# Kernel optimization log

Measured on AMD Instinct MI355X. Metric: run time of the kernel, lower is better.

The kernel has to match this reference:

```python
import jax, jax.numpy as jnp
import numpy as np

# ---- config (matches init_kwargs) ----
B, N_ENC, COND_REPEAT = 4, 4, 200
BLOCKS, LAYERS_PER = 2, 8
R, S, CC, CLASSES = 128, 128, 64, 256
Q_ZERO = 128
DILATIONS = [2 ** i for i in range(LAYERS_PER)] * BLOCKS  # [1..128, 1..128]
L = len(DILATIONS)


def setup_inputs() -> dict:
    key = jax.random.key(0)
    ks = jax.random.split(key, 12)
    g = lambda k, shape, fan: (jax.random.normal(k, shape, jnp.float32) / np.float32(np.sqrt(fan)))
    return {
        "encodings": jax.random.normal(ks[0], (B, CC, N_ENC), jnp.float32),
        "W_first": g(ks[1], (R, 1, 2), 2.0),            # causal conv 1->R, k=2
        "b_first": jnp.zeros((R,), jnp.float32),
        "Wc": g(ks[2], (L, 2 * R, R, 2), 2.0 * R),       # dilated causal convs R->2R, k=2
        "bc": jnp.zeros((L, 2 * R), jnp.float32),
        "Wcond": g(ks[3], (L, 2 * R, CC), CC),           # per-layer 1x1 cond (no bias)
        "Wres": g(ks[4], (L, R, R), R),                  # per-layer 1x1 residual
        "bres": jnp.zeros((L, R), jnp.float32),
        "Wskip_l": g(ks[5], (L, S, R), R),               # per-layer 1x1 skip
        "bskip_l": jnp.zeros((L, S), jnp.float32),
        "Wskip0": g(ks[6], (S, R), R),                   # top skip_conv
        "bskip0": jnp.zeros((S,), jnp.float32),
        "Wcond_top": g(ks[7], (S, CC), CC),              # top 1x1 cond (no bias)
        "Wfc": g(ks[8], (S, S), S),
        "bfc": jnp.zeros((S,), jnp.float32),
        "Wlogits": g(ks[9], (CLASSES, S), S),
        "blogits": jnp.zeros((CLASSES,), jnp.float32),
    }


def reference(encodings, W_first, b_first, Wc, bc, Wcond, Wres, bres,
              Wskip_l, bskip_l, Wskip0, bskip0, Wcond_top, Wfc, bfc,
              Wlogits, blogits):
    """Autoregressive WaveNet generation with per-layer dilated-conv queues.
    Returns per-step logits [B, CLASSES, T] (sampling uses argmax, method='max')."""
    T = N_ENC * COND_REPEAT
    # each encoding frame conditions cond_repeat consecutive samples
    c_seq = jnp.repeat(encodings, COND_REPEAT, axis=2).transpose(2, 0, 1)  # [T,B,CC]

    def step(carry, c_t):
        sample, fq, queues = carry  # sample:[B] int, fq:[B] (first-conv queue), queues: tuple of [B,R,d_l]
        x = sample.astype(jnp.float32) / 127.5 - 1.0  # mu-law index -> [-1, 1]
        # first causal conv (k=2): past value from queue, current value x
        res = fq[:, None] * W_first[:, 0, 0] + x[:, None] * W_first[:, 0, 1] + b_first  # [B,R]
        skip = res @ Wskip0.T + bskip0  # [B,S]
        new_queues = []
        for l in range(L):  # fixed structural loop over layers
            q = queues[l]  # [B,R,d_l]; q[:,:,0] is the input from d_l steps ago
            z = q[:, :, 0] @ Wc[l, :, :, 0].T + res @ Wc[l, :, :, 1].T + bc[l]  # [B,2R]
            z = z + c_t @ Wcond[l].T
            gate, out = jnp.split(z, 2, axis=1)
            h = jax.nn.sigmoid(gate) * jnp.tanh(out)
            new_queues.append(jnp.concatenate([q[:, :, 1:], res[:, :, None]], axis=2))
            skip = skip + h @ Wskip_l[l].T + bskip_l[l]
            res = res + h @ Wres[l].T + bres[l]  # residual connection
        s = jax.nn.relu(skip) @ Wfc.T + bfc + c_t @ Wcond_top.T
        logits = jax.nn.relu(s) @ Wlogits.T + blogits  # [B,CLASSES]
        new_sample = jnp.argmax(logits, axis=1).astype(jnp.int32)
        return (new_sample, x, tuple(new_queues)), logits

    carry0 = (jnp.full((B,), Q_ZERO, jnp.int32),
              jnp.zeros((B,), jnp.float32),
              tuple(jnp.zeros((B, R, d), jnp.float32) for d in DILATIONS))
    _, logits = jax.lax.scan(step, carry0, c_seq)
    return logits.transpose(1, 2, 0)  # [B, CLASSES, T]
```

## Files before the change

kernel.cpp:

```cpp
#include <hip/hip_runtime.h>


typedef unsigned long long u64;
typedef float f32x4 __attribute__((ext_vector_type(4)));

#define TSTEPS 800
#define CREP 200

#define CTR_OFF 0
#define ABT_OFF 64
#define RESBOX_OFF 4096
#define BOXB 16384
#define SKIPBOX_OFF (RESBOX_OFF + 4 * BOXB)
#define RING_OFF (SKIPBOX_OFF + 4 * BOXB)
#define RINGB 261120
#define WS_END (RING_OFF + 4 * RINGB)

#define SPIN_LIMIT 1048576

static __device__ __forceinline__ void pub64(u64* p, float x, unsigned tag) {
  const u64 v = (u64)__float_as_uint(x) | ((u64)tag << 32);
  asm volatile("global_atomic_swap_x2 %0, %1, off" ::"v"(p), "v"(v) : "memory");
}
static __device__ __forceinline__ u64 poll64(u64* p) {
  u64 old;
  const u64 z = 0;
  asm volatile("global_atomic_add_x2 %0, %1, %2, off sc0\n\ts_waitcnt vmcnt(0)"
               : "=&v"(old) : "v"(p), "v"(z) : "memory");
  return old;
}
static __device__ __forceinline__ void poll4(u64* p, u64& a, u64& b, u64& c, u64& d) {
  const u64 z = 0;
  asm volatile(
      "global_atomic_add_x2 %0, %4, %5, off sc0\n\t"
      "global_atomic_add_x2 %1, %4, %5, off offset:1024 sc0\n\t"
      "global_atomic_add_x2 %2, %4, %5, off offset:2048 sc0\n\t"
      "global_atomic_add_x2 %3, %4, %5, off offset:3072 sc0\n\t"
      "s_waitcnt vmcnt(0)"
      : "=&v"(a), "=&v"(b), "=&v"(c), "=&v"(d)
      : "v"(p), "v"(z)
      : "memory");
}
static __device__ __forceinline__ unsigned ld32(const unsigned* p) {
  return __hip_atomic_load(p, __ATOMIC_RELAXED, __HIP_MEMORY_SCOPE_AGENT);
}
static __device__ __forceinline__ void st32(unsigned* p, unsigned v) {
  __hip_atomic_store(p, v, __ATOMIC_RELAXED, __HIP_MEMORY_SCOPE_AGENT);
}
static __device__ __forceinline__ float spinf(u64* p, unsigned tag, unsigned* abt) {
  int g = 0;
  for (;;) {
    const u64 v = poll64(p);
    if ((unsigned)(v >> 32) == tag) return __uint_as_float((unsigned)v);
    if (((++g) & 255) == 0) {
      if (g > SPIN_LIMIT || ld32(abt)) { st32(abt, 1u); return 0.f; }
    }
  }
}

__global__ void wn_init(unsigned char* ws) {
  uint4 z; z.x = 0; z.y = 0; z.z = 0; z.w = 0;
  uint4* p = (uint4*)ws;
  const int n = WS_END / 16;
  for (int i = blockIdx.x * blockDim.x + threadIdx.x; i < n; i += gridDim.x * blockDim.x)
    p[i] = z;
}

__global__ __launch_bounds__(512, 2) void wn_main(
    const float* __restrict__ enc, const float* __restrict__ Wfirst,
    const float* __restrict__ bfirst, const float* __restrict__ Wc,
    const float* __restrict__ bcv, const float* __restrict__ Wcond,
    const float* __restrict__ Wres, const float* __restrict__ bres,
    const float* __restrict__ Wskip, const float* __restrict__ bskipl,
    const float* __restrict__ Wskip0, const float* __restrict__ bskip0,
    const float* __restrict__ Wct, const float* __restrict__ Wfcw,
    const float* __restrict__ bfc, const float* __restrict__ Wlg,
    const float* __restrict__ blgg, float* __restrict__ dout,
    unsigned char* __restrict__ ws) {
  __shared__ __attribute__((aligned(16))) float wc0L[32768];
  __shared__ __attribute__((aligned(16))) unsigned char smem[14336];
  float* zbS = (float*)smem;
  float* ct2 = (float*)smem;
  float* resS = (float*)(smem + 4096);
  float* zpartS = (float*)(smem + 4608);
  float* ppS = (float*)(smem + 6656);
  float* hS = (float*)(smem + 8704);
  float* rpartS = (float*)(smem + 9216);
  float* skpartS = (float*)(smem + 11264);
  float* pastS = (float*)(smem + 13312);
  float* amaxv = (float*)(smem + 13824);
  int* amaxi = (int*)(smem + 13840);
  int* argixS = (int*)(smem + 13856);
  int* roleS = (int*)(smem + 13872);

  const int tid = threadIdx.x;
  unsigned* abt = (unsigned*)(ws + ABT_OFF);

  if (tid == 0) {
    unsigned xcc;
    asm volatile("s_getreg_b32 %0, hwreg(HW_REG_XCC_ID)" : "=s"(xcc));
    int role = 999;
    if (xcc < 4)
      role = (int)__hip_atomic_fetch_add((unsigned*)(ws + CTR_OFF) + xcc, 1u,
                                         __ATOMIC_RELAXED, __HIP_MEMORY_SCOPE_AGENT);
    roleS[0] = role;
    roleS[1] = (int)xcc;
  }
  __syncthreads();
  const int role = roleS[0];
  const int b = roleS[1];
  if (role >= 17) return;

  const int jz = tid & 255, kh = tid >> 8;
  const int j3 = tid & 127, q3 = tid >> 7;

  if (role < 16) {
    const int l = role;
    const int dl = 1 << (l & 7);
    const int pfx = (l < 8) ? ((1 << l) - 1) : (254 + (1 << (l - 8)));

    f32x4 wc1h[16];
    f32x4 wresq[8];
    {
      const f32x4* wbase = (const f32x4*)(Wc + ((size_t)(l * 256 + jz) * 128 + kh * 64) * 2);
#pragma unroll
      for (int m = 0; m < 16; m++) {
        const f32x4 v0 = wbase[2 * m];
        const f32x4 v1 = wbase[2 * m + 1];
        f32x4 w1;
        w1.x = v0.y; w1.y = v0.w; w1.z = v1.y; w1.w = v1.w;
        wc1h[m] = w1;
      }
      const f32x4* rbase = (const f32x4*)(Wres + (size_t)(l * 128 + j3) * 128 + q3 * 32);
#pragma unroll
      for (int m = 0; m < 8; m++) wresq[m] = rbase[m];
#pragma unroll
      for (int m = 0; m < 16; m++) asm volatile("" : "+v"(wc1h[m]));
#pragma unroll
      for (int m = 0; m < 8; m++) asm volatile("" : "+v"(wresq[m]));
    }
    const float bresv = bres[l * 128 + j3];

    for (int idx = tid; idx < 32768; idx += 512) {
      const int j = idx >> 7, k = idx & 127;
      wc0L[k * 256 + j] = Wc[((size_t)(l * 256 + j) * 128 + k) * 2];
    }

    if (tid < 256) {
      for (int e = 0; e < 4; e++) {
        float a = bcv[l * 256 + tid];
        for (int c = 0; c < 64; c++)
          a = fmaf(enc[(b * 64 + c) * 4 + e], Wcond[((size_t)l * 256 + tid) * 64 + c], a);
        zbS[e * 256 + tid] = a;
      }
    }
    ppS[tid] = 0.f;

    u64* inbox = (u64*)(ws + RESBOX_OFF + (size_t)b * BOXB) + l * 128;
    u64* outbox = (u64*)(ws + RESBOX_OFF + (size_t)b * BOXB) + ((l + 1) & 15) * 128;
    u64* skipbox = (u64*)(ws + SKIPBOX_OFF + (size_t)b * BOXB) + l * 128;
    float* ringf = (float*)(ws + RING_OFF + (size_t)b * RINGB) + pfx * 128;
    const f32x4* wskb = (const f32x4*)(Wskip + (size_t)(l * 128 + j3) * 128 + q3 * 32);
    __syncthreads();

    for (int t = 0; t < TSTEPS; t++) {
      const unsigned want = (unsigned)(t + 1);
      const int e = t / CREP;

      if (tid < 128) resS[tid] = spinf(inbox + tid, want, abt);
      __syncthreads();

      {
        const f32x4* r4 = (const f32x4*)(resS + kh * 64);
        float zp = 0.f;
#pragma unroll
        for (int m = 0; m < 16; m++) {
          const f32x4 r = r4[m];
          const f32x4 w = wc1h[m];
          zp = fmaf(r.x, w.x, zp);
          zp = fmaf(r.y, w.y, zp);
          zp = fmaf(r.z, w.z, zp);
          zp = fmaf(r.w, w.w, zp);
        }
        zpartS[(kh << 8) | jz] = zp;
      }
      __syncthreads();
      if (tid < 128) {
        const float g0 = zpartS[tid] + zpartS[256 + tid] + ppS[tid] + ppS[256 + tid] +
                         zbS[e * 256 + tid];
        const float o0 = zpartS[128 + tid] + zpartS[384 + tid] + ppS[128 + tid] +
                         ppS[384 + tid] + zbS[e * 256 + 128 + tid];
        hS[tid] = (1.f / (1.f + expf(-g0))) * tanhf(o0);
      }
      __syncthreads();

      {
        const f32x4* h4 = (const f32x4*)(hS + q3 * 32);
        float rp2 = 0.f;
#pragma unroll
        for (int m = 0; m < 8; m++) {
          const f32x4 hv = h4[m];
          const f32x4 w = wresq[m];
          rp2 = fmaf(hv.x, w.x, rp2);
          rp2 = fmaf(hv.y, w.y, rp2);
          rp2 = fmaf(hv.z, w.z, rp2);
          rp2 = fmaf(hv.w, w.w, rp2);
        }
        rpartS[(q3 << 7) | j3] = rp2;
      }
      __syncthreads();
      if (l < 15 && tid < 128)
        pub64(outbox + tid,
              resS[tid] + rpartS[tid] + rpartS[128 + tid] + rpartS[256 + tid] +
                  rpartS[384 + tid] + bresv,
              want);

      {
        const f32x4* h4 = (const f32x4*)(hS + q3 * 32);
        float sp = 0.f;
#pragma unroll
        for (int m = 0; m < 8; m++) {
          const f32x4 wv = wskb[m];
          const f32x4 hv = h4[m];
          sp = fmaf(wv.x, hv.x, sp);
          sp = fmaf(wv.y, hv.y, sp);
          sp = fmaf(wv.z, hv.z, sp);
          sp = fmaf(wv.w, hv.w, sp);
        }
        skpartS[(q3 << 7) | j3] = sp;
      }
      __syncthreads();
      if (tid < 128)
        pub64(skipbox + tid,
              skpartS[tid] + skpartS[128 + tid] + skpartS[256 + tid] + skpartS[384 + tid],
              want);

      if (tid < 128) {
        ringf[(t % dl) * 128 + tid] = resS[tid];
        pastS[tid] = (dl == 1) ? resS[tid] : ringf[((t + 1) % dl) * 128 + tid];
      }
      __syncthreads();
      {
        float ppn = 0.f;
        const int kbase = kh * 64;
#pragma unroll 16
        for (int kk = 0; kk < 64; kk++)
          ppn = fmaf(pastS[kbase + kk], wc0L[(kbase + kk) * 256 + jz], ppn);
        ppS[(kh << 8) | jz] = ppn;
      }
    }
  } else {
    f32x4 wlgr[16], wfcr[8], wsk0[8];
    {
      const f32x4* lb = (const f32x4*)(Wlg + (size_t)jz * 128 + kh * 64);
#pragma unroll
      for (int m = 0; m < 16; m++) wlgr[m] = lb[m];
      const f32x4* fb = (const f32x4*)(Wfcw + (size_t)j3 * 128 + q3 * 32);
      const f32x4* sb = (const f32x4*)(Wskip0 + (size_t)j3 * 128 + q3 * 32);
#pragma unroll
      for (int m = 0; m < 8; m++) {
        wfcr[m] = fb[m];
        wsk0[m] = sb[m];
      }
    }
    float wf0 = 0.f, wf1 = 0.f, bfv = 0.f, bs0 = 0.f, bsum = 0.f, bfcv = 0.f;
    if (tid < 128) {
      wf0 = Wfirst[2 * tid]; wf1 = Wfirst[2 * tid + 1]; bfv = bfirst[tid];
      bs0 = bskip0[tid];
      for (int l2 = 0; l2 < 16; l2++) bsum += bskipl[l2 * 128 + tid];
      bfcv = bfc[tid];
      for (int e = 0; e < 4; e++) {
        float a = 0.f;
        for (int c = 0; c < 64; c++)
          a = fmaf(enc[(b * 64 + c) * 4 + e], Wct[tid * 64 + c], a);
        ct2[e * 128 + tid] = a;
      }
    }
    const float blgv = (tid < 256) ? blgg[tid] : 0.f;
    float fq = 0.f, x = 128.f / 127.5f - 1.f;
    u64* res0box = (u64*)(ws + RESBOX_OFF + (size_t)b * BOXB);
    u64* skb = (u64*)(ws + SKIPBOX_OFF + (size_t)b * BOXB);
    float* res0S = resS;
    float* partS = zpartS;
    float* lgS = ppS;
    float* skS = hS;
    float* s1S = rpartS;
    __syncthreads();

    for (int t = 0; t < TSTEPS; t++) {
      const unsigned want = (unsigned)(t + 1);
      const int e = t / CREP;

      if (tid < 128) {
        const float rv = fmaf(fq, wf0, fmaf(x, wf1, bfv));
        pub64(res0box + tid, rv, want);
        res0S[tid] = rv;
      }
      __syncthreads();

      {
        const f32x4* r4 = (const f32x4*)(res0S + q3 * 32);
        float sp = 0.f;
#pragma unroll
        for (int m = 0; m < 8; m++) {
          const f32x4 rv = r4[m];
          const f32x4 w = wsk0[m];
          sp = fmaf(rv.x, w.x, sp);
          sp = fmaf(rv.y, w.y, sp);
          sp = fmaf(rv.z, w.z, sp);
          sp = fmaf(rv.w, w.w, sp);
        }
        partS[tid] = sp;
      }
      __syncthreads();
      if (tid < 128) {
        float sacc = partS[tid] + partS[128 + tid] + partS[256 + tid] + partS[384 + tid] +
                     bs0 + bsum;
        u64 v[16];
        int g = 0;
        for (;;) {
          bool ok = true;
#pragma unroll
          for (int grp = 0; grp < 4; grp++)
            poll4(skb + grp * 512 + tid, v[grp * 4], v[grp * 4 + 1], v[grp * 4 + 2],
                  v[grp * 4 + 3]);
#pragma unroll
          for (int l2 = 0; l2 < 16; l2++) ok &= ((unsigned)(v[l2] >> 32) == want);
          if (ok) break;
          if (((++g) & 63) == 0) {
            if (g > (SPIN_LIMIT >> 6) || ld32(abt)) { st32(abt, 1u); break; }
          }
        }
#pragma unroll
        for (int l2 = 0; l2 < 16; l2++) sacc += __uint_as_float((unsigned)v[l2]);
        skS[tid] = fmaxf(sacc, 0.f);
      }
      __syncthreads();

      {
        const f32x4* s4 = (const f32x4*)(skS + q3 * 32);
        float p = 0.f;
#pragma unroll
        for (int m = 0; m < 8; m++) {
          const f32x4 sv = s4[m];
          const f32x4 w = wfcr[m];
          p = fmaf(sv.x, w.x, p);
          p = fmaf(sv.y, w.y, p);
          p = fmaf(sv.z, w.z, p);
          p = fmaf(sv.w, w.w, p);
        }
        partS[tid] = p;
      }
      __syncthreads();
      if (tid < 128)
        s1S[tid] = fmaxf(partS[tid] + partS[128 + tid] + partS[256 + tid] +
                             partS[384 + tid] + bfcv + ct2[e * 128 + tid],
                         0.f);
      __syncthreads();

      {
        const f32x4* s4 = (const f32x4*)(s1S + kh * 64);
        float p = 0.f;
#pragma unroll
        for (int m = 0; m < 16; m++) {
          const f32x4 sv = s4[m];
          const f32x4 w = wlgr[m];
          p = fmaf(sv.x, w.x, p);
          p = fmaf(sv.y, w.y, p);
          p = fmaf(sv.z, w.z, p);
          p = fmaf(sv.w, w.w, p);
        }
        lgS[(kh << 8) | jz] = p;
      }
      __syncthreads();

      float lg = 0.f;
      if (tid < 256) lg = lgS[tid] + lgS[256 + tid] + blgv;

      {
        float bv = lg;
        int bi = tid;
#pragma unroll
        for (int off = 32; off >= 1; off >>= 1) {
          const float ov = __shfl_down(bv, (unsigned)off);
          const int oi = __shfl_down(bi, (unsigned)off);
          if (ov > bv || (ov == bv && oi < bi)) { bv = ov; bi = oi; }
        }
        if (tid < 256 && (tid & 63) == 0) { amaxv[tid >> 6] = bv; amaxi[tid >> 6] = bi; }
      }
      __syncthreads();
      if (tid == 0) {
        float bb = amaxv[0];
        int ii = amaxi[0];
        for (int w2 = 1; w2 < 4; w2++)
          if (amaxv[w2] > bb || (amaxv[w2] == bb && amaxi[w2] < ii)) {
            bb = amaxv[w2]; ii = amaxi[w2];
          }
        argixS[0] = ii;
      }
      __syncthreads();
      fq = x;
      x = (float)argixS[0] / 127.5f - 1.f;

      if (tid < 256) dout[((size_t)b * 256 + tid) * TSTEPS + t] = lg;
    }
  }
}

extern "C" void kernel_launch(void* const* d_in, const int* in_sizes, int n_in,
                              void* d_out, int out_size, void* d_ws, size_t ws_size,
                              hipStream_t stream) {
  (void)in_sizes; (void)n_in; (void)out_size; (void)ws_size;
  wn_init<<<256, 256, 0, stream>>>((unsigned char*)d_ws);
  wn_main<<<1024, 512, 0, stream>>>(
      (const float*)d_in[0], (const float*)d_in[1], (const float*)d_in[2],
      (const float*)d_in[3], (const float*)d_in[4], (const float*)d_in[5],
      (const float*)d_in[6], (const float*)d_in[7], (const float*)d_in[8],
      (const float*)d_in[9], (const float*)d_in[10], (const float*)d_in[11],
      (const float*)d_in[12], (const float*)d_in[13], (const float*)d_in[14],
      (const float*)d_in[15], (const float*)d_in[16],
      (float*)d_out, (unsigned char*)d_ws);
}
```

Measured before the change: 24.84 ms.

## Cut per-step barriers in layer blocks by fusing residual/skip GEMVs and keeping past partials in registers

```diff
diff --git a/kernel.cpp b/kernel.cpp
--- a/kernel.cpp
+++ b/kernel.cpp
@@ -29,17 +29,19 @@
                : "=&v"(old) : "v"(p), "v"(z) : "memory");
   return old;
 }
-static __device__ __forceinline__ void poll4(u64* p, u64& a, u64& b, u64& c, u64& d) {
+static __device__ __forceinline__ void poll4nw(u64* p, u64& a, u64& b, u64& c, u64& d) {
   const u64 z = 0;
   asm volatile(
       "global_atomic_add_x2 %0, %4, %5, off sc0\n\t"
       "global_atomic_add_x2 %1, %4, %5, off offset:1024 sc0\n\t"
       "global_atomic_add_x2 %2, %4, %5, off offset:2048 sc0\n\t"
-      "global_atomic_add_x2 %3, %4, %5, off offset:3072 sc0\n\t"
-      "s_waitcnt vmcnt(0)"
+      "global_atomic_add_x2 %3, %4, %5, off offset:3072 sc0"
       : "=&v"(a), "=&v"(b), "=&v"(c), "=&v"(d)
       : "v"(p), "v"(z)
       : "memory");
+}
+static __device__ __forceinline__ void vmwait0() {
+  asm volatile("s_waitcnt vmcnt(0)" ::: "memory");
 }
 static __device__ __forceinline__ unsigned ld32(const unsigned* p) {
   return __hip_atomic_load(p, __ATOMIC_RELAXED, __HIP_MEMORY_SCOPE_AGENT);
@@ -83,7 +85,7 @@
   float* ct2 = (float*)smem;
   float* resS = (float*)(smem + 4096);
   float* zpartS = (float*)(smem + 4608);
-  float* ppS = (float*)(smem + 6656);
+  float* lgS = (float*)(smem + 6656);
   float* hS = (float*)(smem + 8704);
   float* rpartS = (float*)(smem + 9216);
   float* skpartS = (float*)(smem + 11264);
@@ -142,8 +144,8 @@
     const float bresv = bres[l * 128 + j3];
 
     for (int idx = tid; idx < 32768; idx += 512) {
-      const int j = idx >> 7, k = idx & 127;
-      wc0L[k * 256 + j] = Wc[((size_t)(l * 256 + j) * 128 + k) * 2];
+      const int k = idx >> 8, j = idx & 255;
+      wc0L[idx] = Wc[((size_t)(l * 256 + j) * 128 + k) * 2];
     }
 
     if (tid < 256) {
@@ -154,7 +156,7 @@
         zbS[e * 256 + tid] = a;
       }
     }
-    ppS[tid] = 0.f;
+    float ppn = 0.f;
 
     u64* inbox = (u64*)(ws + RESBOX_OFF + (size_t)b * BOXB) + l * 128;
     u64* outbox = (u64*)(ws + RESBOX_OFF + (size_t)b * BOXB) + ((l + 1) & 15) * 128;
@@ -172,7 +174,7 @@
 
       {
         const f32x4* r4 = (const f32x4*)(resS + kh * 64);
-        float zp = 0.f;
+        float zp = ppn;
 #pragma unroll
         for (int m = 0; m < 16; m++) {
           const f32x4 r = r4[m];
@@ -185,68 +187,56 @@
         zpartS[(kh << 8) | jz] = zp;
       }
       __syncthreads();
+
       if (tid < 128) {
-        const float g0 = zpartS[tid] + zpartS[256 + tid] + ppS[tid] + ppS[256 + tid] +
-                         zbS[e * 256 + tid];
-        const float o0 = zpartS[128 + tid] + zpartS[384 + tid] + ppS[128 + tid] +
-                         ppS[384 + tid] + zbS[e * 256 + 128 + tid];
+        const float g0 = zpartS[tid] + zpartS[256 + tid] + zbS[e * 256 + tid];
+        const float o0 = zpartS[128 + tid] + zpartS[384 + tid] + zbS[e * 256 + 128 + tid];
         hS[tid] = (1.f / (1.f + expf(-g0))) * tanhf(o0);
+        ringf[(t % dl) * 128 + tid] = resS[tid];
+        pastS[tid] = (dl == 1) ? resS[tid] : ringf[((t + 1) % dl) * 128 + tid];
       }
       __syncthreads();
 
       {
         const f32x4* h4 = (const f32x4*)(hS + q3 * 32);
-        float rp2 = 0.f;
+        float rp2 = 0.f, sp = 0.f;
 #pragma unroll
         for (int m = 0; m < 8; m++) {
           const f32x4 hv = h4[m];
-          const f32x4 w = wresq[m];
-          rp2 = fmaf(hv.x, w.x, rp2);
-          rp2 = fmaf(hv.y, w.y, rp2);
-          rp2 = fmaf(hv.z, w.z, rp2);
-          rp2 = fmaf(hv.w, w.w, rp2);
+          const f32x4 wr = wresq[m];
+          const f32x4 wk = wskb[m];
+          rp2 = fmaf(hv.x, wr.x, rp2);
+          rp2 = fmaf(hv.y, wr.y, rp2);
+          rp2 = fmaf(hv.z, wr.z, rp2);
+          rp2 = fmaf(hv.w, wr.w, rp2);
+          sp = fmaf(hv.x, wk.x, sp);
+          sp = fmaf(hv.y, wk.y, sp);
+          sp = fmaf(hv.z, wk.z, sp);
+          sp = fmaf(hv.w, wk.w, sp);
         }
         rpartS[(q3 << 7) | j3] = rp2;
-      }
-      __syncthreads();
-      if (l < 15 && tid < 128)
-        pub64(outbox + tid,
-              resS[tid] + rpartS[tid] + rpartS[128 + tid] + rpartS[256 + tid] +
-                  rpartS[384 + tid] + bresv,
-              want);
-
-      {
-        const f32x4* h4 = (const f32x4*)(hS + q3 * 32);
-        float sp = 0.f;
-#pragma unroll
-        for (int m = 0; m < 8; m++) {
-          const f32x4 wv = wskb[m];
-          const f32x4 hv = h4[m];
-          sp = fmaf(wv.x, hv.x, sp);
-          sp = fmaf(wv.y, hv.y, sp);
-          sp = fmaf(wv.z, hv.z, sp);
-          sp = fmaf(wv.w, hv.w, sp);
-        }
         skpartS[(q3 << 7) | j3] = sp;
       }
       __syncthreads();
-      if (tid < 128)
+
+      if (tid < 128) {
+        if (l < 15)
+          pub64(outbox + tid,
+                resS[tid] + rpartS[tid] + rpartS[128 + tid] + rpartS[256 + tid] +
+                    rpartS[384 + tid] + bresv,
+                want);
         pub64(skipbox + tid,
               skpartS[tid] + skpartS[128 + tid] + skpartS[256 + tid] + skpartS[384 + tid],
               want);
-
-      if (tid < 128) {
-        ringf[(t % dl) * 128 + tid] = resS[tid];
-        pastS[tid] = (dl == 1) ? resS[tid] : ringf[((t + 1) % dl) * 128 + tid];
-      }
-      __syncthreads();
-      {
-        float ppn = 0.f;
+      }
+
+      {
+        float p2 = 0.f;
         const int kbase = kh * 64;
 #pragma unroll 16
         for (int kk = 0; kk < 64; kk++)
-          ppn = fmaf(pastS[kbase + kk], wc0L[(kbase + kk) * 256 + jz], ppn);
-        ppS[(kh << 8) | jz] = ppn;
+          p2 = fmaf(pastS[kbase + kk], wc0L[(kbase + kk) * 256 + jz], p2);
+        ppn = p2;
       }
     }
   } else {
@@ -282,7 +272,6 @@
     u64* skb = (u64*)(ws + SKIPBOX_OFF + (size_t)b * BOXB);
     float* res0S = resS;
     float* partS = zpartS;
-    float* lgS = ppS;
     float* skS = hS;
     float* s1S = rpartS;
     __syncthreads();
@@ -320,10 +309,11 @@
         int g = 0;
         for (;;) {
           bool ok = true;
-#pragma unroll
-          for (int grp = 0; grp < 4; grp++)
-            poll4(skb + grp * 512 + tid, v[grp * 4], v[grp * 4 + 1], v[grp * 4 + 2],
-                  v[grp * 4 + 3]);
+          poll4nw(skb + 0 * 512 + tid, v[0], v[1], v[2], v[3]);
+          poll4nw(skb + 1 * 512 + tid, v[4], v[5], v[6], v[7]);
+          poll4nw(skb + 2 * 512 + tid, v[8], v[9], v[10], v[11]);
+          poll4nw(skb + 3 * 512 + tid, v[12], v[13], v[14], v[15]);
+          vmwait0();
 #pragma unroll
           for (int l2 = 0; l2 < 16; l2++) ok &= ((unsigned)(v[l2] >> 32) == want);
           if (ok) break;
```

New measurement: 45.41 ms. 82.9% more time.
